# Optimization experiments

Measured on AMD Instinct MI355X. Metric: run time of the kernel, lower is better.

## Reference

```python
import jax, jax.numpy as jnp
import numpy as np

B, M, N, P, H, W, D, DIMG, NH = 32, 2048, 512, 16, 640, 640, 256, 384, 8
PD = 3 * P * P  # 768 flattened patch dim


def layer_norm(x, g, b, eps=1e-5):
    mu = x.mean(-1, keepdims=True)
    var = ((x - mu) ** 2).mean(-1, keepdims=True)
    return (x - mu) * jax.lax.rsqrt(var + eps) * g + b


def get_patches(img, kpts, patch):
    # img [B,3,H,W], kpts [B,N,2] (x,y), NaN rows -> NaN patches
    Bb, C, Hh, Ww = img.shape
    half = patch // 2
    safe = jnp.nan_to_num(kpts, nan=0.0)
    ctr = jnp.round(safe).astype(jnp.int32)
    x0 = jnp.clip(ctr[..., 0] - half, 0, Ww - patch)
    y0 = jnp.clip(ctr[..., 1] - half, 0, Hh - patch)
    offs = jnp.arange(patch)
    ys = y0[..., None] + offs  # [B,N,P]
    xs = x0[..., None] + offs  # [B,N,P]

    def ext(im_b, ys_b, xs_b):
        p = im_b[:, ys_b[:, :, None], xs_b[:, None, :]]  # [C,N,P,P]
        return jnp.transpose(p, (1, 0, 2, 3))  # [N,C,P,P]

    patches = jax.vmap(ext)(img, ys, xs)  # [B,N,C,P,P]
    invalid = jnp.isnan(kpts).any(-1)
    return jnp.where(invalid[:, :, None, None, None], jnp.nan, patches)


def setup_inputs() -> dict:
    key = jax.random.key(0)
    ks = jax.random.split(key, 16)
    im0 = jax.random.uniform(ks[0], (B, 3, H, W), jnp.float32)
    im1 = jax.random.uniform(ks[1], (B, 3, H, W), jnp.float32)
    wh = jnp.array([W - 1.0, H - 1.0], jnp.float32)
    kpts0 = jax.random.uniform(ks[2], (B, M, 2), jnp.float32) * wh
    kpts1 = jax.random.uniform(ks[3], (B, M, 2), jnp.float32) * wh
    scores0 = jax.random.uniform(ks[4], (B, M), jnp.float32)
    scores1 = jax.random.uniform(ks[5], (B, M), jnp.float32)
    image_embs = jax.random.normal(ks[6], (B, DIMG), jnp.float32)
    m0 = jax.random.randint(ks[7], (B, N), 0, M)
    m1 = jax.random.randint(ks[8], (B, N), -300, M)
    m1 = jnp.where(m1 < 0, -1, m1)
    sorted_matches = jnp.stack([m0, m1], axis=-1).astype(jnp.int32)
    s = 0.02
    params = dict(
        ln1_g=jnp.ones((PD,), jnp.float32), ln1_b=jnp.zeros((PD,), jnp.float32),
        W_pe=jax.random.normal(ks[9], (D - 1, PD), jnp.float32) * s,
        b_pe=jnp.zeros((D - 1,), jnp.float32),
        ln2_g=jnp.ones((D - 1,), jnp.float32), ln2_b=jnp.zeros((D - 1,), jnp.float32),
        W_proj=jax.random.normal(ks[10], (D, DIMG), jnp.float32) * s,
        b_proj=jnp.zeros((D,), jnp.float32),
        in_w=jax.random.normal(ks[11], (3 * D, D), jnp.float32) * s,
        in_b=jnp.zeros((3 * D,), jnp.float32),
        out_w=jax.random.normal(ks[12], (D, D), jnp.float32) * s,
        out_b=jnp.zeros((D,), jnp.float32),
        W_fc=jax.random.normal(ks[13], (6, D), jnp.float32) * s,
        b_fc=jnp.zeros((6,), jnp.float32),
    )
    return dict(im0=im0, im1=im1, kpts0=kpts0, kpts1=kpts1, scores0=scores0,
                scores1=scores1, image_embs=image_embs,
                sorted_matches=sorted_matches, **params)


def reference(im0, im1, kpts0, kpts1, scores0, scores1, image_embs,
              sorted_matches, ln1_g, ln1_b, W_pe, b_pe, ln2_g, ln2_b,
              W_proj, b_proj, in_w, in_b, out_w, out_b, W_fc, b_fc):
    im0 = jnp.clip(im0, 0.0, 1.0)
    im1 = jnp.clip(im1, 0.0, 1.0)
    m0 = sorted_matches[..., 0]
    m1 = sorted_matches[..., 1]
    valid = m1 > -1  # [B,N]
    m0c = jnp.clip(m0, 0, M - 1)
    m1c = jnp.clip(m1, 0, M - 1)
    # vectorized masked gather with NaN padding (replaces the double python loop)
    g0 = jnp.take_along_axis(kpts0, m0c[..., None], axis=1)  # [B,N,2]
    g1 = jnp.take_along_axis(kpts1, m1c[..., None], axis=1)
    k0v = jnp.where(valid[..., None], g0, jnp.nan)
    k1v = jnp.where(valid[..., None], g1, jnp.nan)
    s0v = jnp.where(valid, jnp.take_along_axis(scores0, m0c, axis=1), 0.0)
    s1v = jnp.where(valid, jnp.take_along_axis(scores1, m1c, axis=1), 0.0)
    p0 = jnp.nan_to_num(get_patches(im0, k0v, P), nan=-1.0)  # [B,N,3,P,P]
    p1 = jnp.nan_to_num(get_patches(im1, k1v, P), nan=-1.0)
    patches = jnp.concatenate([p0, p1], axis=1)  # [B,2N,3,P,P]
    flat = patches.reshape(B, 2 * N, PD)
    e = layer_norm(flat, ln1_g, ln1_b)
    e = e @ W_pe.T + b_pe
    e = layer_norm(e, ln2_g, ln2_b)  # [B,2N,D-1]
    scores = jnp.concatenate([s0v, s1v], axis=1)  # [B,2N]
    pe = jnp.concatenate([e, scores[..., None]], axis=-1)  # [B,2N,D]
    # motion estimator: cross-attn, query = projected image embedding
    q = image_embs @ W_proj.T + b_proj  # [B,D]
    Wq, Wk, Wv = in_w[:D], in_w[D:2 * D], in_w[2 * D:]
    bq, bk, bv = in_b[:D], in_b[D:2 * D], in_b[2 * D:]
    dh = D // NH
    qh = (q @ Wq.T + bq).reshape(B, 1, NH, dh)
    kh = (pe @ Wk.T + bk).reshape(B, 2 * N, NH, dh)
    vh = (pe @ Wv.T + bv).reshape(B, 2 * N, NH, dh)
    scale = 1.0 / np.sqrt(dh).astype(np.float32)
    att = jnp.einsum('bqhd,bkhd->bhqk', qh, kh) * scale
    a = jax.nn.softmax(att, axis=-1)
    o = jnp.einsum('bhqk,bkhd->bqhd', a, vh).reshape(B, 1, D)
    o = o @ out_w.T + out_b
    out = (o @ W_fc.T + b_fc).reshape(B, 6)
    return out
```

## Files before the change

### kernel.cpp

```cpp
#include <hip/hip_runtime.h>
#include <math.h>

#define BB 32
#define MM 2048
#define NN 512
#define PSZ 16
#define HH 640
#define WW 640
#define DD 256
#define DIMG_ 384
#define NHEADS 8
#define PD_ 768
#define TWO_N 1024
#define ROWS_TOT (BB * TWO_N)

typedef short bf16x8 __attribute__((ext_vector_type(8)));
typedef float f32x4  __attribute__((ext_vector_type(4)));

__device__ __forceinline__ unsigned short f2bf(float x) {
  unsigned int u = __float_as_uint(x);
  u = (u + 0x7FFF + ((u >> 16) & 1)) >> 16;
  return (unsigned short)u;
}
__device__ __forceinline__ float bf2f(unsigned short h) {
  return __uint_as_float(((unsigned int)h) << 16);
}

__device__ __forceinline__ void gload_lds16(const void* g, void* l) {
  __builtin_amdgcn_global_load_lds(
      (const __attribute__((address_space(1))) void*)g,
      (__attribute__((address_space(3))) void*)l, 16, 0, 0);
}

__global__ __launch_bounds__(256) void qproj_kernel(
    const float* __restrict__ image_embs,
    const float* __restrict__ W_proj, const float* __restrict__ b_proj,
    const float* __restrict__ in_w,   const float* __restrict__ in_b,
    float* __restrict__ u_out, float* __restrict__ bias_out)
{
  __shared__ float q1[DD];
  __shared__ float q2[DD];
  const int t = threadIdx.x;
  const int b = blockIdx.x;

  {
    const float* emb = image_embs + (size_t)b * DIMG_;
    const float* wr  = W_proj + (size_t)t * DIMG_;
    float a = b_proj[t];
    for (int i = 0; i < DIMG_; ++i) a += emb[i] * wr[i];
    q1[t] = a;
  }
  __syncthreads();
  {
    const float* wr = in_w + (size_t)t * DD;
    float a = in_b[t];
    for (int i = 0; i < DD; ++i) a += q1[i] * wr[i];
    q2[t] = a;
  }
  __syncthreads();
  #pragma unroll
  for (int h = 0; h < NHEADS; ++h) {
    float s = 0.0f;
    #pragma unroll 8
    for (int i = 0; i < 32; ++i)
      s += q2[h * 32 + i] * in_w[(size_t)(DD + h * 32 + i) * DD + t];
    u_out[((size_t)b * NHEADS + h) * DD + t] = s;
  }
  if (t < NHEADS) {
    float s = 0.0f;
    for (int i = 0; i < 32; ++i) s += q2[t * 32 + i] * in_b[DD + t * 32 + i];
    bias_out[b * NHEADS + t] = s;
  }
}

__global__ __launch_bounds__(256) void wconv_kernel(
    const float* __restrict__ W_pe,
    unsigned short* __restrict__ Whi, unsigned short* __restrict__ Wlo)
{
  const int idx = blockIdx.x * 256 + threadIdx.x;
  const int row = idx / PD_;
  float v = (row < 255) ? W_pe[idx] : 0.0f;
  const unsigned short h = f2bf(v);
  Whi[idx] = h;
  Wlo[idx] = f2bf(v - bf2f(h));
}

__global__ __launch_bounds__(256) void extract_kernel(
    const float* __restrict__ im0, const float* __restrict__ im1,
    const float* __restrict__ kpts0, const float* __restrict__ kpts1,
    const float* __restrict__ scores0, const float* __restrict__ scores1,
    const int*   __restrict__ sorted_matches,
    const float* __restrict__ ln1_g, const float* __restrict__ ln1_b,
    unsigned short* __restrict__ Ahi, unsigned short* __restrict__ Alo,
    float* __restrict__ score_all)
{
  __shared__ __align__(16) float A[16][PD_];
  __shared__ int   sx0[16], sy0[16], svalid[16];
  __shared__ float smu[16], srs[16];

  const int t   = threadIdx.x;
  const int blk = blockIdx.x;
  const int b      = blk >> 6;
  const int n2base = (blk & 63) << 4;
  const bool side1 = (n2base >= NN);
  const float* img  = side1 ? im1 : im0;
  const float* kpts = side1 ? kpts1 : kpts0;
  const float* scrs = side1 ? scores1 : scores0;

  if (t < 16) {
    const int n2 = n2base + t;
    const int n  = side1 ? (n2 - NN) : n2;
    const int m0 = sorted_matches[((size_t)b * NN + n) * 2 + 0];
    const int m1 = sorted_matches[((size_t)b * NN + n) * 2 + 1];
    const int valid = (m1 > -1) ? 1 : 0;
    int midx = side1 ? m1 : m0;
    midx = min(max(midx, 0), MM - 1);
    const float kx = kpts[((size_t)b * MM + midx) * 2 + 0];
    const float ky = kpts[((size_t)b * MM + midx) * 2 + 1];
    const int cx = (int)rintf(kx);
    const int cy = (int)rintf(ky);
    sx0[t] = min(max(cx - 8, 0), WW - PSZ);
    sy0[t] = min(max(cy - 8, 0), HH - PSZ);
    svalid[t] = valid;
    score_all[blk * 16 + t] = valid ? scrs[(size_t)b * MM + midx] : 0.0f;
  }
  __syncthreads();

  const size_t imb = (size_t)b * 3 * HH * WW;
  #pragma unroll 4
  for (int i = 0; i < 48; ++i) {
    const int idx = i * 256 + t;
    const int p   = idx / PD_;
    const int rem = idx - p * PD_;
    const int c   = rem >> 8;
    const int r2  = rem & 255;
    const int py  = r2 >> 4;
    const int px  = r2 & 15;
    float v = -1.0f;
    if (svalid[p]) {
      const float pix = img[imb + ((size_t)c * HH + (sy0[p] + py)) * WW + sx0[p] + px];
      v = fminf(fmaxf(pix, 0.0f), 1.0f);
    }
    A[p][rem] = v;
  }
  __syncthreads();

  {
    const int p = t >> 4, j = t & 15;
    float s = 0.0f, ss = 0.0f;
    #pragma unroll 8
    for (int i = 0; i < 48; ++i) { const float v = A[p][j + 16 * i]; s += v; ss += v * v; }
    #pragma unroll
    for (int m = 8; m; m >>= 1) { s += __shfl_xor(s, m, 16); ss += __shfl_xor(ss, m, 16); }
    if (j == 0) {
      const float mu  = s * (1.0f / 768.0f);
      const float var = ss * (1.0f / 768.0f) - mu * mu;
      smu[p] = mu;
      srs[p] = 1.0f / sqrtf(var + 1e-5f);
    }
  }
  __syncthreads();

  #pragma unroll 4
  for (int i = 0; i < 48; ++i) {
    const int idx = i * 256 + t;
    const int p   = idx / PD_;
    const int rem = idx - p * PD_;
    const float y = (A[p][rem] - smu[p]) * srs[p] * ln1_g[rem] + ln1_b[rem];
    const size_t o = (size_t)(blk * 16 + p) * PD_ + rem;
    const unsigned short h = f2bf(y);
    Ahi[o] = h;
    Alo[o] = f2bf(y - bf2f(h));
  }
}

__global__ __launch_bounds__(256) void gemm_pe_kernel(
    const unsigned short* __restrict__ Ahi, const unsigned short* __restrict__ Alo,
    const unsigned short* __restrict__ Whi, const unsigned short* __restrict__ Wlo,
    float* __restrict__ e)
{
  __shared__ __align__(16) unsigned short As[2][128][32];
  __shared__ __align__(16) unsigned short Bs[2][128][32];

  const int t  = threadIdx.x;
  const int w  = t >> 6;
  const int L  = t & 63;
  const int mt = blockIdx.x >> 1;
  const int nt = blockIdx.x & 1;

  f32x4 acc[4][4];
  #pragma unroll
  for (int i = 0; i < 4; ++i)
    #pragma unroll
    for (int j = 0; j < 4; ++j) acc[i][j] = (f32x4){0.f, 0.f, 0.f, 0.f};

  const unsigned short* src;
  unsigned short* dstbase;
  long rowbase;
  if      (w == 0) { src = Ahi; dstbase = &As[0][0][0]; rowbase = (long)mt * 128; }
  else if (w == 1) { src = Alo; dstbase = &As[1][0][0]; rowbase = (long)mt * 128; }
  else if (w == 2) { src = Whi; dstbase = &Bs[0][0][0]; rowbase = (long)nt * 128; }
  else             { src = Wlo; dstbase = &Bs[1][0][0]; rowbase = (long)nt * 128; }
  const int rr   = L >> 2;
  const int q_st = (L & 3) ^ ((L >> 4) & 3);

  const int lane_m = L & 15;
  const int quad   = L >> 4;
  const int swz    = quad ^ (lane_m >> 2);

  const unsigned short* As0 = &As[0][0][0];
  const unsigned short* As1 = &As[1][0][0];
  const unsigned short* Bs0 = &Bs[0][0][0];
  const unsigned short* Bs1 = &Bs[1][0][0];
  const int am0 = (w >> 1) * 64;
  const int bn0 = (w & 1) * 64;

  for (int ks = 0; ks < PD_ / 32; ++ks) {
    const int k0 = ks * 32;
    __syncthreads();
    {
      const unsigned short* gs = src + (rowbase + rr) * (long)PD_ + k0 + q_st * 8;
      #pragma unroll
      for (int c = 0; c < 8; ++c)
        gload_lds16(gs + (long)c * 16 * PD_, dstbase + c * 512);
    }
    __syncthreads();

    bf16x8 ah[4], al[4], bh[4], bl[4];
    #pragma unroll
    for (int i = 0; i < 4; ++i) {
      const int offa = (am0 + i * 16 + lane_m) * 32 + swz * 8;
      ah[i] = *(const bf16x8*)(As0 + offa);
      al[i] = *(const bf16x8*)(As1 + offa);
      const int offb = (bn0 + i * 16 + lane_m) * 32 + swz * 8;
      bh[i] = *(const bf16x8*)(Bs0 + offb);
      bl[i] = *(const bf16x8*)(Bs1 + offb);
    }
    #pragma unroll
    for (int i = 0; i < 4; ++i)
      #pragma unroll
      for (int j = 0; j < 4; ++j) {
        acc[i][j] = __builtin_amdgcn_mfma_f32_16x16x32_bf16(ah[i], bh[j], acc[i][j], 0, 0, 0);
        acc[i][j] = __builtin_amdgcn_mfma_f32_16x16x32_bf16(ah[i], bl[j], acc[i][j], 0, 0, 0);
        acc[i][j] = __builtin_amdgcn_mfma_f32_16x16x32_bf16(al[i], bh[j], acc[i][j], 0, 0, 0);
      }
  }

  const long grow0 = (long)mt * 128 + am0;
  const int  gcol0 = nt * 128 + bn0;
  #pragma unroll
  for (int i = 0; i < 4; ++i)
    #pragma unroll
    for (int j = 0; j < 4; ++j)
      #pragma unroll
      for (int v = 0; v < 4; ++v) {
        const long row = grow0 + i * 16 + quad * 4 + v;
        const int  col = gcol0 + j * 16 + lane_m;
        e[row * DD + col] = acc[i][j][v];
      }
}

__global__ __launch_bounds__(256) void ln2_logits_kernel(
    float* epe,
    const float* __restrict__ b_pe,
    const float* __restrict__ ln2_g, const float* __restrict__ ln2_b,
    const float* __restrict__ score_all,
    const float* __restrict__ u, const float* __restrict__ ubias,
    float* __restrict__ lt)
{
  const int t = threadIdx.x;
  const int g = t >> 5, l = t & 31;
  const long row = (long)blockIdx.x * 8 + g;
  const int  b   = (int)(row >> 10);
  float* er = epe + row * DD;

  float x[8];
  float s = 0.0f, ss = 0.0f;
  #pragma unroll
  for (int j = 0; j < 8; ++j) {
    const int c = l + 32 * j;
    float v = er[c];
    if (c < 255) { v += b_pe[c]; s += v; ss += v * v; }
    x[j] = v;
  }
  #pragma unroll
  for (int m = 16; m; m >>= 1) { s += __shfl_xor(s, m, 32); ss += __shfl_xor(ss, m, 32); }
  const float mu  = s * (1.0f / 255.0f);
  const float var = ss * (1.0f / 255.0f) - mu * mu;
  const float rs  = 1.0f / sqrtf(var + 1e-5f);

  float y[8];
  #pragma unroll
  for (int j = 0; j < 8; ++j) {
    const int c = l + 32 * j;
    y[j] = (c < 255) ? (x[j] - mu) * rs * ln2_g[c] + ln2_b[c] : score_all[row];
    er[c] = y[j];
  }

  const float* ub = u + (size_t)b * NHEADS * DD;
  float d[NHEADS] = {0, 0, 0, 0, 0, 0, 0, 0};
  #pragma unroll
  for (int j = 0; j < 8; ++j) {
    const int c = l + 32 * j;
    #pragma unroll
    for (int h = 0; h < NHEADS; ++h) d[h] += y[j] * ub[h * DD + c];
  }
  #pragma unroll
  for (int h = 0; h < NHEADS; ++h) {
    #pragma unroll
    for (int m = 16; m; m >>= 1) d[h] += __shfl_xor(d[h], m, 32);
  }
  if (l == 0) {
    const float sc = 0.17677669529663687f;
    #pragma unroll
    for (int h = 0; h < NHEADS; ++h)
      lt[row * NHEADS + h] = (d[h] + ubias[b * NHEADS + h]) * sc;
  }
}

__global__ __launch_bounds__(256) void softmax_kernel(float* __restrict__ lt)
{
  const int b = blockIdx.x, t = threadIdx.x;
  const int h = t >> 5, l = t & 31;
  float* base = lt + (size_t)b * TWO_N * NHEADS + h;
  float v[32];
  float mx = -1e30f;
  #pragma unroll 8
  for (int i = 0; i < 32; ++i) { v[i] = base[(l + 32 * i) * NHEADS]; mx = fmaxf(mx, v[i]); }
  #pragma unroll
  for (int m = 16; m; m >>= 1) mx = fmaxf(mx, __shfl_xor(mx, m, 32));
  float sm = 0.0f;
  #pragma unroll 8
  for (int i = 0; i < 32; ++i) { v[i] = expf(v[i] - mx); sm += v[i]; }
  #pragma unroll
  for (int m = 16; m; m >>= 1) sm += __shfl_xor(sm, m, 32);
  const float inv = 1.0f / sm;
  #pragma unroll 8
  for (int i = 0; i < 32; ++i) base[(l + 32 * i) * NHEADS] = v[i] * inv;
}

__global__ __launch_bounds__(256) void ctx_kernel(
    const float* __restrict__ pe, const float* __restrict__ lt,
    float* __restrict__ ctxp)
{
  const int b = blockIdx.x, ch = blockIdx.y, t = threadIdx.x;
  const float* peb = pe + ((size_t)b * TWO_N + ch * 128) * DD;
  const float* ab  = lt + ((size_t)b * TWO_N + ch * 128) * NHEADS;
  float acc[NHEADS] = {0, 0, 0, 0, 0, 0, 0, 0};
  for (int k = 0; k < 128; ++k) {
    const float v = peb[(size_t)k * DD + t];
    const float4 a0 = *(const float4*)(ab + k * NHEADS);
    const float4 a1 = *(const float4*)(ab + k * NHEADS + 4);
    acc[0] += a0.x * v; acc[1] += a0.y * v; acc[2] += a0.z * v; acc[3] += a0.w * v;
    acc[4] += a1.x * v; acc[5] += a1.y * v; acc[6] += a1.z * v; acc[7] += a1.w * v;
  }
  #pragma unroll
  for (int h = 0; h < NHEADS; ++h)
    ctxp[(((size_t)b * 8 + ch) * NHEADS + h) * DD + t] = acc[h];
}

__global__ __launch_bounds__(256) void final_kernel(
    const float* __restrict__ ctxp,
    const float* __restrict__ in_w,  const float* __restrict__ in_b,
    const float* __restrict__ out_w, const float* __restrict__ out_b,
    const float* __restrict__ W_fc,  const float* __restrict__ b_fc,
    float* __restrict__ outp)
{
  __shared__ float ctx_sh[NHEADS * DD];
  __shared__ float o_sh[DD], o2_sh[DD];
  const int t = threadIdx.x;
  const int b = blockIdx.x;

  #pragma unroll
  for (int h = 0; h < NHEADS; ++h) {
    float s = 0.0f;
    #pragma unroll
    for (int ch = 0; ch < 8; ++ch)
      s += ctxp[(((size_t)b * 8 + ch) * NHEADS + h) * DD + t];
    ctx_sh[h * DD + t] = s;
  }
  __syncthreads();
  {
    const float* wv = in_w + (size_t)(2 * DD + t) * DD;
    const float* cx = ctx_sh + (t >> 5) * DD;
    float o1 = in_b[2 * DD + t];
    for (int j = 0; j < DD; ++j) o1 += wv[j] * cx[j];
    o_sh[t] = o1;
  }
  __syncthreads();
  {
    const float* wr = out_w + (size_t)t * DD;
    float o2 = out_b[t];
    for (int j = 0; j < DD; ++j) o2 += wr[j] * o_sh[j];
    o2_sh[t] = o2;
  }
  __syncthreads();
  if (t < 6) {
    const float* wr = W_fc + (size_t)t * DD;
    float r = b_fc[t];
    for (int j = 0; j < DD; ++j) r += wr[j] * o2_sh[j];
    outp[b * 6 + t] = r;
  }
}

extern "C" void kernel_launch(void* const* d_in, const int* in_sizes, int n_in,
                              void* d_out, int out_size, void* d_ws, size_t ws_size,
                              hipStream_t stream) {
  const float* im0       = (const float*)d_in[0];
  const float* im1       = (const float*)d_in[1];
  const float* kpts0     = (const float*)d_in[2];
  const float* kpts1     = (const float*)d_in[3];
  const float* scores0   = (const float*)d_in[4];
  const float* scores1   = (const float*)d_in[5];
  const float* image_embs= (const float*)d_in[6];
  const int*   smatch    = (const int*)d_in[7];
  const float* ln1_g     = (const float*)d_in[8];
  const float* ln1_b     = (const float*)d_in[9];
  const float* W_pe      = (const float*)d_in[10];
  const float* b_pe      = (const float*)d_in[11];
  const float* ln2_g     = (const float*)d_in[12];
  const float* ln2_b     = (const float*)d_in[13];
  const float* W_proj    = (const float*)d_in[14];
  const float* b_proj    = (const float*)d_in[15];
  const float* in_w      = (const float*)d_in[16];
  const float* in_b      = (const float*)d_in[17];
  const float* out_w     = (const float*)d_in[18];
  const float* out_b     = (const float*)d_in[19];
  const float* W_fc      = (const float*)d_in[20];
  const float* b_fc      = (const float*)d_in[21];

  char* ws = (char*)d_ws;
  size_t off = 0;
  float* epe   = (float*)(ws + off); off += (size_t)ROWS_TOT * DD * 4;
  float* u     = (float*)(ws + off); off += (size_t)BB * NHEADS * DD * 4;
  float* ubias = (float*)(ws + off); off += (size_t)BB * NHEADS * 4;
  off = (off + 1023) & ~(size_t)1023;
  float* score = (float*)(ws + off); off += (size_t)ROWS_TOT * 4;
  float* lt    = (float*)(ws + off); off += (size_t)BB * TWO_N * NHEADS * 4;
  float* ctxp  = (float*)(ws + off); off += (size_t)BB * 8 * NHEADS * DD * 4;
  unsigned short* Whi = (unsigned short*)(ws + off); off += (size_t)256 * PD_ * 2;
  unsigned short* Wlo = (unsigned short*)(ws + off); off += (size_t)256 * PD_ * 2;
  off = (off + 1023) & ~(size_t)1023;
  unsigned short* Ahi = (unsigned short*)(ws + off); off += (size_t)ROWS_TOT * PD_ * 2;
  unsigned short* Alo = (unsigned short*)(ws + off); off += (size_t)ROWS_TOT * PD_ * 2;

  qproj_kernel<<<BB, 256, 0, stream>>>(image_embs, W_proj, b_proj, in_w, in_b,
                                       u, ubias);
  wconv_kernel<<<(256 * PD_) / 256, 256, 0, stream>>>(W_pe, Whi, Wlo);
  extract_kernel<<<ROWS_TOT / 16, 256, 0, stream>>>(
      im0, im1, kpts0, kpts1, scores0, scores1, smatch,
      ln1_g, ln1_b, Ahi, Alo, score);
  gemm_pe_kernel<<<(ROWS_TOT / 128) * 2, 256, 0, stream>>>(Ahi, Alo, Whi, Wlo, epe);
  ln2_logits_kernel<<<ROWS_TOT / 8, 256, 0, stream>>>(
      epe, b_pe, ln2_g, ln2_b, score, u, ubias, lt);
  softmax_kernel<<<BB, 256, 0, stream>>>(lt);
  ctx_kernel<<<dim3(BB, 8), 256, 0, stream>>>(epe, lt, ctxp);
  final_kernel<<<BB, 256, 0, stream>>>(ctxp, in_w, in_b, out_w, out_b,
                                       W_fc, b_fc, (float*)d_out);
}
```

Baseline: 562.5 us.

## Merge prep kernels, rework patch extraction per wavefront, fuse softmax into ctx

Merges weight conversion and query projection into one launch, and moves softmax into the context kernel, where each block recomputes the softmax for its batch into shared memory. Patch extraction now uses one wavefront per patch with register-held values, wave-level LayerNorm reductions and paired 32-bit bf16 stores, which removes the LDS staging and block barriers. The GEMM block index is remapped so consecutive blocks share A tiles across both N tiles. Small GEMV loops are vectorised with float4. The cost is redundant softmax work across the 8 ctx blocks per batch.

```diff
diff --git a/kernel.cpp b/kernel.cpp
--- a/kernel.cpp
+++ b/kernel.cpp
@@ -32,7 +32,9 @@
       (__attribute__((address_space(3))) void*)l, 16, 0, 0);
 }
 
-__global__ __launch_bounds__(256) void qproj_kernel(
+__global__ __launch_bounds__(256) void prep_kernel(
+    const float* __restrict__ W_pe,
+    unsigned short* __restrict__ Whi, unsigned short* __restrict__ Wlo,
     const float* __restrict__ image_embs,
     const float* __restrict__ W_proj, const float* __restrict__ b_proj,
     const float* __restrict__ in_w,   const float* __restrict__ in_b,
@@ -41,20 +43,39 @@
   __shared__ float q1[DD];
   __shared__ float q2[DD];
   const int t = threadIdx.x;
-  const int b = blockIdx.x;
-
+
+  if (blockIdx.x < 768) {
+    const int idx = blockIdx.x * 256 + t;
+    const int row = idx / PD_;
+    float v = (row < 255) ? W_pe[idx] : 0.0f;
+    const unsigned short h = f2bf(v);
+    Whi[idx] = h;
+    Wlo[idx] = f2bf(v - bf2f(h));
+    return;
+  }
+
+  const int b = blockIdx.x - 768;
   {
-    const float* emb = image_embs + (size_t)b * DIMG_;
-    const float* wr  = W_proj + (size_t)t * DIMG_;
+    const float4* emb = (const float4*)(image_embs + (size_t)b * DIMG_);
+    const float4* wr  = (const float4*)(W_proj + (size_t)t * DIMG_);
     float a = b_proj[t];
-    for (int i = 0; i < DIMG_; ++i) a += emb[i] * wr[i];
+    #pragma unroll 4
+    for (int i = 0; i < DIMG_ / 4; ++i) {
+      const float4 e4 = emb[i], w4 = wr[i];
+      a += e4.x * w4.x + e4.y * w4.y + e4.z * w4.z + e4.w * w4.w;
+    }
     q1[t] = a;
   }
   __syncthreads();
   {
-    const float* wr = in_w + (size_t)t * DD;
+    const float4* wr = (const float4*)(in_w + (size_t)t * DD);
+    const float4* qq = (const float4*)q1;
     float a = in_b[t];
-    for (int i = 0; i < DD; ++i) a += q1[i] * wr[i];
+    #pragma unroll 4
+    for (int i = 0; i < DD / 4; ++i) {
+      const float4 q4 = qq[i], w4 = wr[i];
+      a += q4.x * w4.x + q4.y * w4.y + q4.z * w4.z + q4.w * w4.w;
+    }
     q2[t] = a;
   }
   __syncthreads();
@@ -71,18 +92,6 @@
     for (int i = 0; i < 32; ++i) s += q2[t * 32 + i] * in_b[DD + t * 32 + i];
     bias_out[b * NHEADS + t] = s;
   }
-}
-
-__global__ __launch_bounds__(256) void wconv_kernel(
-    const float* __restrict__ W_pe,
-    unsigned short* __restrict__ Whi, unsigned short* __restrict__ Wlo)
-{
-  const int idx = blockIdx.x * 256 + threadIdx.x;
-  const int row = idx / PD_;
-  float v = (row < 255) ? W_pe[idx] : 0.0f;
-  const unsigned short h = f2bf(v);
-  Whi[idx] = h;
-  Wlo[idx] = f2bf(v - bf2f(h));
 }
 
 __global__ __launch_bounds__(256) void extract_kernel(
@@ -94,83 +103,69 @@
     unsigned short* __restrict__ Ahi, unsigned short* __restrict__ Alo,
     float* __restrict__ score_all)
 {
-  __shared__ __align__(16) float A[16][PD_];
-  __shared__ int   sx0[16], sy0[16], svalid[16];
-  __shared__ float smu[16], srs[16];
-
-  const int t   = threadIdx.x;
-  const int blk = blockIdx.x;
-  const int b      = blk >> 6;
-  const int n2base = (blk & 63) << 4;
-  const bool side1 = (n2base >= NN);
+  const int t  = threadIdx.x;
+  const int L  = t & 63;
+  const long gp = (long)blockIdx.x * 4 + (t >> 6);
+  const int b   = (int)(gp >> 10);
+  const int n2  = (int)(gp & 1023);
+  const bool side1 = (n2 >= NN);
   const float* img  = side1 ? im1 : im0;
   const float* kpts = side1 ? kpts1 : kpts0;
   const float* scrs = side1 ? scores1 : scores0;
 
-  if (t < 16) {
-    const int n2 = n2base + t;
-    const int n  = side1 ? (n2 - NN) : n2;
-    const int m0 = sorted_matches[((size_t)b * NN + n) * 2 + 0];
-    const int m1 = sorted_matches[((size_t)b * NN + n) * 2 + 1];
-    const int valid = (m1 > -1) ? 1 : 0;
-    int midx = side1 ? m1 : m0;
-    midx = min(max(midx, 0), MM - 1);
-    const float kx = kpts[((size_t)b * MM + midx) * 2 + 0];
-    const float ky = kpts[((size_t)b * MM + midx) * 2 + 1];
-    const int cx = (int)rintf(kx);
-    const int cy = (int)rintf(ky);
-    sx0[t] = min(max(cx - 8, 0), WW - PSZ);
-    sy0[t] = min(max(cy - 8, 0), HH - PSZ);
-    svalid[t] = valid;
-    score_all[blk * 16 + t] = valid ? scrs[(size_t)b * MM + midx] : 0.0f;
-  }
-  __syncthreads();
-
-  const size_t imb = (size_t)b * 3 * HH * WW;
-  #pragma unroll 4
-  for (int i = 0; i < 48; ++i) {
-    const int idx = i * 256 + t;
-    const int p   = idx / PD_;
-    const int rem = idx - p * PD_;
-    const int c   = rem >> 8;
-    const int r2  = rem & 255;
-    const int py  = r2 >> 4;
-    const int px  = r2 & 15;
-    float v = -1.0f;
-    if (svalid[p]) {
-      const float pix = img[imb + ((size_t)c * HH + (sy0[p] + py)) * WW + sx0[p] + px];
-      v = fminf(fmaxf(pix, 0.0f), 1.0f);
-    }
-    A[p][rem] = v;
-  }
-  __syncthreads();
-
-  {
-    const int p = t >> 4, j = t & 15;
-    float s = 0.0f, ss = 0.0f;
-    #pragma unroll 8
-    for (int i = 0; i < 48; ++i) { const float v = A[p][j + 16 * i]; s += v; ss += v * v; }
-    #pragma unroll
-    for (int m = 8; m; m >>= 1) { s += __shfl_xor(s, m, 16); ss += __shfl_xor(ss, m, 16); }
-    if (j == 0) {
-      const float mu  = s * (1.0f / 768.0f);
-      const float var = ss * (1.0f / 768.0f) - mu * mu;
-      smu[p] = mu;
-      srs[p] = 1.0f / sqrtf(var + 1e-5f);
-    }
-  }
-  __syncthreads();
-
-  #pragma unroll 4
-  for (int i = 0; i < 48; ++i) {
-    const int idx = i * 256 + t;
-    const int p   = idx / PD_;
-    const int rem = idx - p * PD_;
-    const float y = (A[p][rem] - smu[p]) * srs[p] * ln1_g[rem] + ln1_b[rem];
-    const size_t o = (size_t)(blk * 16 + p) * PD_ + rem;
-    const unsigned short h = f2bf(y);
-    Ahi[o] = h;
-    Alo[o] = f2bf(y - bf2f(h));
+  const int n  = side1 ? (n2 - NN) : n2;
+  const int m0 = sorted_matches[((size_t)b * NN + n) * 2 + 0];
+  const int m1 = sorted_matches[((size_t)b * NN + n) * 2 + 1];
+  const bool valid = (m1 > -1);
+  int midx = side1 ? m1 : m0;
+  midx = min(max(midx, 0), MM - 1);
+  const float kx = kpts[((size_t)b * MM + midx) * 2 + 0];
+  const float ky = kpts[((size_t)b * MM + midx) * 2 + 1];
+  const int x0 = min(max((int)rintf(kx) - 8, 0), WW - PSZ);
+  const int y0 = min(max((int)rintf(ky) - 8, 0), HH - PSZ);
+
+  float v[12];
+  if (valid) {
+    const size_t imb = (size_t)b * 3 * HH * WW;
+    const int px = (2 * L) & 15;
+    #pragma unroll
+    for (int j = 0; j < 6; ++j) {
+      const int p0 = 2 * L + 128 * j;
+      const int c  = p0 >> 8;
+      const int py = (p0 >> 4) & 15;
+      const float* rp = img + imb + ((size_t)c * HH + y0 + py) * WW + x0 + px;
+      v[2 * j]     = fminf(fmaxf(rp[0], 0.0f), 1.0f);
+      v[2 * j + 1] = fminf(fmaxf(rp[1], 0.0f), 1.0f);
+    }
+  } else {
+    #pragma unroll
+    for (int i = 0; i < 12; ++i) v[i] = -1.0f;
+  }
+
+  float s = 0.0f, ss = 0.0f;
+  #pragma unroll
+  for (int i = 0; i < 12; ++i) { s += v[i]; ss += v[i] * v[i]; }
+  #pragma unroll
+  for (int m = 32; m; m >>= 1) { s += __shfl_xor(s, m); ss += __shfl_xor(ss, m); }
+  const float mu  = s * (1.0f / 768.0f);
+  const float var = ss * (1.0f / 768.0f) - mu * mu;
+  const float rs  = 1.0f / sqrtf(var + 1e-5f);
+
+  unsigned int* AhiW = (unsigned int*)(Ahi + gp * PD_);
+  unsigned int* AloW = (unsigned int*)(Alo + gp * PD_);
+  #pragma unroll
+  for (int j = 0; j < 6; ++j) {
+    const int p0 = 2 * L + 128 * j;
+    const float y0e = (v[2 * j]     - mu) * rs * ln1_g[p0]     + ln1_b[p0];
+    const float y1e = (v[2 * j + 1] - mu) * rs * ln1_g[p0 + 1] + ln1_b[p0 + 1];
+    const unsigned short h0 = f2bf(y0e), h1 = f2bf(y1e);
+    AhiW[p0 >> 1] = (unsigned int)h0 | ((unsigned int)h1 << 16);
+    const unsigned short l0 = f2bf(y0e - bf2f(h0));
+    const unsigned short l1 = f2bf(y1e - bf2f(h1));
+    AloW[p0 >> 1] = (unsigned int)l0 | ((unsigned int)l1 << 16);
+  }
+  if (L == 0) {
+    score_all[gp] = valid ? scrs[(size_t)b * MM + midx] : 0.0f;
   }
 }
 
@@ -185,8 +180,9 @@
   const int t  = threadIdx.x;
   const int w  = t >> 6;
   const int L  = t & 63;
-  const int mt = blockIdx.x >> 1;
-  const int nt = blockIdx.x & 1;
+  const int id = blockIdx.x;
+  const int nt = (id >> 3) & 1;
+  const int mt = ((id >> 4) << 3) | (id & 7);
 
   f32x4 acc[4][4];
   #pragma unroll
@@ -318,39 +314,39 @@
   }
 }
 
-__global__ __launch_bounds__(256) void softmax_kernel(float* __restrict__ lt)
-{
-  const int b = blockIdx.x, t = threadIdx.x;
-  const int h = t >> 5, l = t & 31;
-  float* base = lt + (size_t)b * TWO_N * NHEADS + h;
-  float v[32];
-  float mx = -1e30f;
-  #pragma unroll 8
-  for (int i = 0; i < 32; ++i) { v[i] = base[(l + 32 * i) * NHEADS]; mx = fmaxf(mx, v[i]); }
-  #pragma unroll
-  for (int m = 16; m; m >>= 1) mx = fmaxf(mx, __shfl_xor(mx, m, 32));
-  float sm = 0.0f;
-  #pragma unroll 8
-  for (int i = 0; i < 32; ++i) { v[i] = expf(v[i] - mx); sm += v[i]; }
-  #pragma unroll
-  for (int m = 16; m; m >>= 1) sm += __shfl_xor(sm, m, 32);
-  const float inv = 1.0f / sm;
-  #pragma unroll 8
-  for (int i = 0; i < 32; ++i) base[(l + 32 * i) * NHEADS] = v[i] * inv;
-}
-
 __global__ __launch_bounds__(256) void ctx_kernel(
     const float* __restrict__ pe, const float* __restrict__ lt,
     float* __restrict__ ctxp)
 {
+  __shared__ __align__(16) float pr[TWO_N][NHEADS];
   const int b = blockIdx.x, ch = blockIdx.y, t = threadIdx.x;
+
+  {
+    const int h = t >> 5, l = t & 31;
+    const float* base = lt + (size_t)b * TWO_N * NHEADS + h;
+    float v[32];
+    float mx = -1e30f;
+    #pragma unroll 8
+    for (int i = 0; i < 32; ++i) { v[i] = base[(l + 32 * i) * NHEADS]; mx = fmaxf(mx, v[i]); }
+    #pragma unroll
+    for (int m = 16; m; m >>= 1) mx = fmaxf(mx, __shfl_xor(mx, m, 32));
+    float sm = 0.0f;
+    #pragma unroll 8
+    for (int i = 0; i < 32; ++i) { v[i] = expf(v[i] - mx); sm += v[i]; }
+    #pragma unroll
+    for (int m = 16; m; m >>= 1) sm += __shfl_xor(sm, m, 32);
+    const float inv = 1.0f / sm;
+    #pragma unroll 8
+    for (int i = 0; i < 32; ++i) pr[l + 32 * i][h] = v[i] * inv;
+  }
+  __syncthreads();
+
   const float* peb = pe + ((size_t)b * TWO_N + ch * 128) * DD;
-  const float* ab  = lt + ((size_t)b * TWO_N + ch * 128) * NHEADS;
   float acc[NHEADS] = {0, 0, 0, 0, 0, 0, 0, 0};
   for (int k = 0; k < 128; ++k) {
     const float v = peb[(size_t)k * DD + t];
-    const float4 a0 = *(const float4*)(ab + k * NHEADS);
-    const float4 a1 = *(const float4*)(ab + k * NHEADS + 4);
+    const float4 a0 = *(const float4*)&pr[ch * 128 + k][0];
+    const float4 a1 = *(const float4*)&pr[ch * 128 + k][4];
     acc[0] += a0.x * v; acc[1] += a0.y * v; acc[2] += a0.z * v; acc[3] += a0.w * v;
     acc[4] += a1.x * v; acc[5] += a1.y * v; acc[6] += a1.z * v; acc[7] += a1.w * v;
   }
@@ -366,8 +362,8 @@
     const float* __restrict__ W_fc,  const float* __restrict__ b_fc,
     float* __restrict__ outp)
 {
-  __shared__ float ctx_sh[NHEADS * DD];
-  __shared__ float o_sh[DD], o2_sh[DD];
+  __shared__ __align__(16) float ctx_sh[NHEADS * DD];
+  __shared__ __align__(16) float o_sh[DD], o2_sh[DD];
   const int t = threadIdx.x;
   const int b = blockIdx.x;
 
@@ -381,24 +377,37 @@
   }
   __syncthreads();
   {
-    const float* wv = in_w + (size_t)(2 * DD + t) * DD;
-    const float* cx = ctx_sh + (t >> 5) * DD;
+    const float4* wv = (const float4*)(in_w + (size_t)(2 * DD + t) * DD);
+    const float4* cx = (const float4*)(ctx_sh + (t >> 5) * DD);
     float o1 = in_b[2 * DD + t];
-    for (int j = 0; j < DD; ++j) o1 += wv[j] * cx[j];
+    #pragma unroll 4
+    for (int j = 0; j < DD / 4; ++j) {
+      const float4 w4 = wv[j], c4 = cx[j];
+      o1 += w4.x * c4.x + w4.y * c4.y + w4.z * c4.z + w4.w * c4.w;
+    }
     o_sh[t] = o1;
   }
   __syncthreads();
   {
-    const float* wr = out_w + (size_t)t * DD;
+    const float4* wr = (const float4*)(out_w + (size_t)t * DD);
+    const float4* oo = (const float4*)o_sh;
     float o2 = out_b[t];
-    for (int j = 0; j < DD; ++j) o2 += wr[j] * o_sh[j];
+    #pragma unroll 4
+    for (int j = 0; j < DD / 4; ++j) {
+      const float4 w4 = wr[j], c4 = oo[j];
+      o2 += w4.x * c4.x + w4.y * c4.y + w4.z * c4.z + w4.w * c4.w;
+    }
     o2_sh[t] = o2;
   }
   __syncthreads();
   if (t < 6) {
-    const float* wr = W_fc + (size_t)t * DD;
+    const float4* wr = (const float4*)(W_fc + (size_t)t * DD);
+    const float4* oo = (const float4*)o2_sh;
     float r = b_fc[t];
-    for (int j = 0; j < DD; ++j) r += wr[j] * o2_sh[j];
+    for (int j = 0; j < DD / 4; ++j) {
+      const float4 w4 = wr[j], c4 = oo[j];
+      r += w4.x * c4.x + w4.y * c4.y + w4.z * c4.z + w4.w * c4.w;
+    }
     outp[b * 6 + t] = r;
   }
 }
@@ -444,16 +453,15 @@
   unsigned short* Ahi = (unsigned short*)(ws + off); off += (size_t)ROWS_TOT * PD_ * 2;
   unsigned short* Alo = (unsigned short*)(ws + off); off += (size_t)ROWS_TOT * PD_ * 2;
 
-  qproj_kernel<<<BB, 256, 0, stream>>>(image_embs, W_proj, b_proj, in_w, in_b,
-                                       u, ubias);
-  wconv_kernel<<<(256 * PD_) / 256, 256, 0, stream>>>(W_pe, Whi, Wlo);
-  extract_kernel<<<ROWS_TOT / 16, 256, 0, stream>>>(
+  prep_kernel<<<768 + BB, 256, 0, stream>>>(W_pe, Whi, Wlo,
+                                            image_embs, W_proj, b_proj,
+                                            in_w, in_b, u, ubias);
+  extract_kernel<<<ROWS_TOT / 4, 256, 0, stream>>>(
       im0, im1, kpts0, kpts1, scores0, scores1, smatch,
       ln1_g, ln1_b, Ahi, Alo, score);
   gemm_pe_kernel<<<(ROWS_TOT / 128) * 2, 256, 0, stream>>>(Ahi, Alo, Whi, Wlo, epe);
   ln2_logits_kernel<<<ROWS_TOT / 8, 256, 0, stream>>>(
       epe, b_pe, ln2_g, ln2_b, score, u, ubias, lt);
-  softmax_kernel<<<BB, 256, 0, stream>>>(lt);
   ctx_kernel<<<dim3(BB, 8), 256, 0, stream>>>(epe, lt, ctxp);
   final_kernel<<<BB, 256, 0, stream>>>(ctxp, in_w, in_b, out_w, out_b,
                                        W_fc, b_fc, (float*)d_out);
```

Result: faster. 494.9 us (-12.0%).
